# Kernel optimization log

Hardware: AMD Instinct MI355X
Metric: run time of the kernel (lower is better)

## Reference

```python
import jax, jax.numpy as jnp
import numpy as np

LUT_N = 16 * 17 * 17 * 17  # 78608, covers max index 16*(16*17*17 + 16*17 + 16) = 78592
H = W = 2048


def setup_inputs() -> dict:
    key = jax.random.key(0)
    k1, k2, k3, k4 = jax.random.split(key, 4)
    # quantized pixel values in [0, 16], stored as float like the torch module expects
    x_in = jax.random.randint(k1, (1, 3, H, W), 0, 17).astype(jnp.float32)
    x_s = jax.random.randint(k2, (1, 3, H, W), 0, 17).astype(jnp.float32)
    # int8 LUT tables of shape [N, 20, 1, 1]
    feature_msb = jax.random.randint(k3, (LUT_N, 20, 1, 1), -32, 32).astype(jnp.int8)
    feature_lsb = jax.random.randint(k4, (LUT_N, 20, 1, 1), -32, 32).astype(jnp.int8)
    return {"x_in": x_in, "x_s": x_s, "feature_msb": feature_msb, "feature_lsb": feature_lsb}


def reference(x_in, x_s, feature_msb, feature_lsb):
    B, C, Hh, Ww = x_in.shape
    # index weights: [16*17*17, 16*17, 16], broadcast over (1,3,1,1)
    weights = jnp.array([16 * 17 * 17, 16 * 17, 16], dtype=jnp.float32).reshape(1, 3, 1, 1)
    idx_msb = jnp.sum(x_in * weights, axis=1).reshape(-1).astype(jnp.int32)  # [B*H*W]
    idx_lsb = jnp.sum(x_s * weights, axis=1).reshape(-1).astype(jnp.int32)
    nfeat = feature_msb.shape[1]  # 20
    # gather -> (1, H, W, 20) -> (1, 20, H, W), cast to float as in torch .float()
    out_msb = feature_msb[idx_msb].reshape(1, Hh, Ww, nfeat).transpose(0, 3, 1, 2).astype(jnp.float32)
    out_lsb = feature_lsb[idx_lsb].reshape(1, Hh, Ww, nfeat).transpose(0, 3, 1, 2).astype(jnp.float32)
    out = out_msb + out_lsb
    # AdaptiveAvgPool2d(1) == global mean over H, W
    out = jnp.mean(out, axis=(2, 3), keepdims=True)  # (1, 20, 1, 1)
    # quantize to 0.25 steps and clamp to [-32, 31.75]
    out = jnp.clip(jnp.round(out * 4.0) / 4.0, -32.0, 31.75)
    return out
```

## Files before the change

kernel.cpp:

```cpp
#include <hip/hip_runtime.h>


#define NBINS 4913
#define NPIX  (2048 * 2048)
#define G4    (NPIX / 4)
#define NFEAT 20

__global__ __launch_bounds__(256) void compact_k(const int* __restrict__ msb,
                                                 const int* __restrict__ lsb,
                                                 int* __restrict__ cm,
                                                 int* __restrict__ cl) {
    int ok = 1;
    for (int i = 0; i < 64; ++i) {
        int v = msb[i];
        ok &= (v >= -32 && v < 32);
    }
    const bool is_int32 = (ok != 0);

    const int total = NBINS * 5;
    int t = blockIdx.x * 256 + threadIdx.x;
    const int stride = gridDim.x * 256;
    for (; t < total; t += stride) {
        int j = t / 5;
        int k = t - j * 5;
        int wm, wl;
        if (is_int32) {
            const int* rm = msb + j * 320 + k * 4;
            const int* rl = lsb + j * 320 + k * 4;
            unsigned um = (unsigned)(rm[0] & 0xff) | ((unsigned)(rm[1] & 0xff) << 8) |
                          ((unsigned)(rm[2] & 0xff) << 16) | ((unsigned)(rm[3] & 0xff) << 24);
            unsigned ul = (unsigned)(rl[0] & 0xff) | ((unsigned)(rl[1] & 0xff) << 8) |
                          ((unsigned)(rl[2] & 0xff) << 16) | ((unsigned)(rl[3] & 0xff) << 24);
            wm = (int)um;
            wl = (int)ul;
        } else {
            wm = msb[j * 80 + k];
            wl = lsb[j * 80 + k];
        }
        cm[t] = wm;
        cl[t] = wl;
    }
}

__global__ __launch_bounds__(256) void feat_main(const float* __restrict__ xin,
                                                 const float* __restrict__ xs,
                                                 const int* __restrict__ cm,
                                                 const int* __restrict__ cl,
                                                 int* __restrict__ partial) {
    __shared__ int hist[NBINS];
    __shared__ int wsum[4][NFEAT];
    for (int i = threadIdx.x; i < NBINS; i += 256) hist[i] = 0;
    __syncthreads();

    const float4* a = (const float4*)xin;
    const float4* b = (const float4*)xs;
    const int nt = gridDim.x * 256;
    for (int g = blockIdx.x * 256 + threadIdx.x; g < G4; g += nt) {
        float4 a0 = a[g], a1 = a[g + G4], a2 = a[g + 2 * G4];
        float4 b0 = b[g], b1 = b[g + G4], b2 = b[g + 2 * G4];

        int m0 = (int)fmaf(a0.x, 289.0f, fmaf(a1.x, 17.0f, a2.x));
        int m1 = (int)fmaf(a0.y, 289.0f, fmaf(a1.y, 17.0f, a2.y));
        int m2 = (int)fmaf(a0.z, 289.0f, fmaf(a1.z, 17.0f, a2.z));
        int m3 = (int)fmaf(a0.w, 289.0f, fmaf(a1.w, 17.0f, a2.w));
        int s0 = (int)fmaf(b0.x, 289.0f, fmaf(b1.x, 17.0f, b2.x));
        int s1 = (int)fmaf(b0.y, 289.0f, fmaf(b1.y, 17.0f, b2.y));
        int s2 = (int)fmaf(b0.z, 289.0f, fmaf(b1.z, 17.0f, b2.z));
        int s3 = (int)fmaf(b0.w, 289.0f, fmaf(b1.w, 17.0f, b2.w));

        atomicAdd(&hist[m0], 1);
        atomicAdd(&hist[m1], 1);
        atomicAdd(&hist[m2], 1);
        atomicAdd(&hist[m3], 1);
        atomicAdd(&hist[s0], 1 << 16);
        atomicAdd(&hist[s1], 1 << 16);
        atomicAdd(&hist[s2], 1 << 16);
        atomicAdd(&hist[s3], 1 << 16);
    }
    __syncthreads();

    int acc[NFEAT];
#pragma unroll
    for (int f = 0; f < NFEAT; ++f) acc[f] = 0;

    for (int j = threadIdx.x; j < NBINS; j += 256) {
        int h = hist[j];
        int hm = h & 0xffff;
        int hl = (int)((unsigned)h >> 16);
        if (hm) {
            const int* r = cm + j * 5;
#pragma unroll
            for (int k = 0; k < 5; ++k) {
                int w = r[k];
                acc[4 * k + 0] += hm * ((w << 24) >> 24);
                acc[4 * k + 1] += hm * ((w << 16) >> 24);
                acc[4 * k + 2] += hm * ((w << 8) >> 24);
                acc[4 * k + 3] += hm * (w >> 24);
            }
        }
        if (hl) {
            const int* r = cl + j * 5;
#pragma unroll
            for (int k = 0; k < 5; ++k) {
                int w = r[k];
                acc[4 * k + 0] += hl * ((w << 24) >> 24);
                acc[4 * k + 1] += hl * ((w << 16) >> 24);
                acc[4 * k + 2] += hl * ((w << 8) >> 24);
                acc[4 * k + 3] += hl * (w >> 24);
            }
        }
    }

    const int lane = threadIdx.x & 63;
    const int wv = threadIdx.x >> 6;
#pragma unroll
    for (int f = 0; f < NFEAT; ++f) {
        int v = acc[f];
#pragma unroll
        for (int o = 32; o > 0; o >>= 1) v += __shfl_xor(v, o, 64);
        if (lane == 0) wsum[wv][f] = v;
    }
    __syncthreads();
    if (threadIdx.x < NFEAT) {
        int f = threadIdx.x;
        partial[blockIdx.x * NFEAT + f] = wsum[0][f] + wsum[1][f] + wsum[2][f] + wsum[3][f];
    }
}

__global__ __launch_bounds__(64) void finalize_k(const int* __restrict__ partial,
                                                 float* __restrict__ out, int nb) {
    const int f = blockIdx.x;
    const int lane = threadIdx.x;
    int s = 0;
    for (int b = lane; b < nb; b += 64) s += partial[b * NFEAT + f];
#pragma unroll
    for (int o = 32; o > 0; o >>= 1) s += __shfl_xor(s, o, 64);
    if (lane == 0) {
        double m4 = (double)s * (1.0 / 1048576.0);
        double r = rint(m4);
        float v = (float)(r * 0.25);
        v = fminf(fmaxf(v, -32.0f), 31.75f);
        out[f] = v;
    }
}

extern "C" void kernel_launch(void* const* d_in, const int* in_sizes, int n_in,
                              void* d_out, int out_size, void* d_ws, size_t ws_size,
                              hipStream_t stream) {
    const float* xin = (const float*)d_in[0];
    const float* xs = (const float*)d_in[1];
    const int* msb = (const int*)d_in[2];
    const int* lsb = (const int*)d_in[3];
    float* out = (float*)d_out;

    int* cm = (int*)d_ws;
    int* cl = (int*)((char*)d_ws + 98304);
    int* partial = (int*)((char*)d_ws + 2 * 98304);

    const int mb = (ws_size >= (size_t)(2 * 98304) + 2048u * NFEAT * 4u) ? 2048 : 1024;

    compact_k<<<96, 256, 0, stream>>>(msb, lsb, cm, cl);
    feat_main<<<mb, 256, 0, stream>>>(xin, xs, cm, cl, partial);
    finalize_k<<<NFEAT, 64, 0, stream>>>(partial, out, mb);
}
```

Before: 169.8 us.

## Merge per-block histograms globally before LUT dot product

Each histogram block now writes its shared-memory histogram to a global workspace row instead of multiplying it against the LUT itself. A separate merge kernel sums the histograms across blocks per bin and does the 20-feature dot product once per bin. This replaces 2048 redundant per-block dot products over 4913 bins with one. The cost is an extra kernel launch and roughly 40 MB of histogram traffic written and read back. The old fused path is kept as a fallback when the workspace is too small.

```diff
diff --git a/kernel.cpp b/kernel.cpp
--- a/kernel.cpp
+++ b/kernel.cpp
@@ -2,9 +2,14 @@
 
 
 #define NBINS 4913
+#define HPAD  4928
 #define NPIX  (2048 * 2048)
 #define G4    (NPIX / 4)
 #define NFEAT 20
+#define MERGE_BLOCKS 154
+
+#define PART_OFF 196608
+#define HIST_OFF 278528
 
 __global__ __launch_bounds__(256) void compact_k(const int* __restrict__ msb,
                                                  const int* __restrict__ lsb,
@@ -42,13 +47,10 @@
     }
 }
 
-__global__ __launch_bounds__(256) void feat_main(const float* __restrict__ xin,
+__global__ __launch_bounds__(256) void feat_hist(const float* __restrict__ xin,
                                                  const float* __restrict__ xs,
-                                                 const int* __restrict__ cm,
-                                                 const int* __restrict__ cl,
-                                                 int* __restrict__ partial) {
+                                                 unsigned* __restrict__ hists) {
     __shared__ int hist[NBINS];
-    __shared__ int wsum[4][NFEAT];
     for (int i = threadIdx.x; i < NBINS; i += 256) hist[i] = 0;
     __syncthreads();
 
@@ -79,10 +81,102 @@
     }
     __syncthreads();
 
+    unsigned* row = hists + (size_t)blockIdx.x * HPAD;
+    for (int i = threadIdx.x; i < HPAD; i += 256)
+        row[i] = (i < NBINS) ? (unsigned)hist[i] : 0u;
+}
+
+__global__ __launch_bounds__(256) void merge_dot_k(const unsigned* __restrict__ hists,
+                                                   const int* __restrict__ cm,
+                                                   const int* __restrict__ cl,
+                                                   int* __restrict__ partial, int nh) {
+    __shared__ unsigned part[8][32];
+    const int t = threadIdx.x;
+    const int s = t >> 5;
+    const int bo = t & 31;
+    const int j = blockIdx.x * 32 + bo;
+
+    unsigned sum = 0;
+    for (int b = s; b < nh; b += 8)
+        sum += hists[(size_t)b * HPAD + j];
+    part[s][bo] = sum;
+    __syncthreads();
+
+    if (t < 32) {
+        unsigned h = 0;
+#pragma unroll
+        for (int ss = 0; ss < 8; ++ss) h += part[ss][bo];
+        int hm = (int)(h & 0xffffu);
+        int hl = (int)(h >> 16);
+
+        int acc[NFEAT];
+#pragma unroll
+        for (int f = 0; f < NFEAT; ++f) acc[f] = 0;
+        if (j < NBINS && h != 0u) {
+            const int* rm = cm + j * 5;
+            const int* rl = cl + j * 5;
+#pragma unroll
+            for (int k = 0; k < 5; ++k) {
+                int wm = rm[k], wl = rl[k];
+                acc[4 * k + 0] += hm * ((wm << 24) >> 24) + hl * ((wl << 24) >> 24);
+                acc[4 * k + 1] += hm * ((wm << 16) >> 24) + hl * ((wl << 16) >> 24);
+                acc[4 * k + 2] += hm * ((wm << 8) >> 24) + hl * ((wl << 8) >> 24);
+                acc[4 * k + 3] += hm * (wm >> 24) + hl * (wl >> 24);
+            }
+        }
+#pragma unroll
+        for (int f = 0; f < NFEAT; ++f) {
+            int v = acc[f];
+#pragma unroll
+            for (int o = 16; o > 0; o >>= 1) v += __shfl_xor(v, o, 64);
+            acc[f] = v;
+        }
+        if (t == 0) {
+#pragma unroll
+            for (int f = 0; f < NFEAT; ++f)
+                partial[blockIdx.x * NFEAT + f] = acc[f];
+        }
+    }
+}
+
+__global__ __launch_bounds__(256) void feat_dot(const float* __restrict__ xin,
+                                                const float* __restrict__ xs,
+                                                const int* __restrict__ cm,
+                                                const int* __restrict__ cl,
+                                                int* __restrict__ partial) {
+    __shared__ int hist[NBINS];
+    __shared__ int wsum[4][NFEAT];
+    for (int i = threadIdx.x; i < NBINS; i += 256) hist[i] = 0;
+    __syncthreads();
+
+    const float4* a = (const float4*)xin;
+    const float4* b = (const float4*)xs;
+    const int nt = gridDim.x * 256;
+    for (int g = blockIdx.x * 256 + threadIdx.x; g < G4; g += nt) {
+        float4 a0 = a[g], a1 = a[g + G4], a2 = a[g + 2 * G4];
+        float4 b0 = b[g], b1 = b[g + G4], b2 = b[g + 2 * G4];
+        int m0 = (int)fmaf(a0.x, 289.0f, fmaf(a1.x, 17.0f, a2.x));
+        int m1 = (int)fmaf(a0.y, 289.0f, fmaf(a1.y, 17.0f, a2.y));
+        int m2 = (int)fmaf(a0.z, 289.0f, fmaf(a1.z, 17.0f, a2.z));
+        int m3 = (int)fmaf(a0.w, 289.0f, fmaf(a1.w, 17.0f, a2.w));
+        int s0 = (int)fmaf(b0.x, 289.0f, fmaf(b1.x, 17.0f, b2.x));
+        int s1 = (int)fmaf(b0.y, 289.0f, fmaf(b1.y, 17.0f, b2.y));
+        int s2 = (int)fmaf(b0.z, 289.0f, fmaf(b1.z, 17.0f, b2.z));
+        int s3 = (int)fmaf(b0.w, 289.0f, fmaf(b1.w, 17.0f, b2.w));
+        atomicAdd(&hist[m0], 1);
+        atomicAdd(&hist[m1], 1);
+        atomicAdd(&hist[m2], 1);
+        atomicAdd(&hist[m3], 1);
+        atomicAdd(&hist[s0], 1 << 16);
+        atomicAdd(&hist[s1], 1 << 16);
+        atomicAdd(&hist[s2], 1 << 16);
+        atomicAdd(&hist[s3], 1 << 16);
+    }
+    __syncthreads();
+
     int acc[NFEAT];
 #pragma unroll
     for (int f = 0; f < NFEAT; ++f) acc[f] = 0;
-
     for (int j = threadIdx.x; j < NBINS; j += 256) {
         int h = hist[j];
         int hm = h & 0xffff;
@@ -155,11 +249,21 @@
 
     int* cm = (int*)d_ws;
     int* cl = (int*)((char*)d_ws + 98304);
-    int* partial = (int*)((char*)d_ws + 2 * 98304);
-
-    const int mb = (ws_size >= (size_t)(2 * 98304) + 2048u * NFEAT * 4u) ? 2048 : 1024;
+    int* partial = (int*)((char*)d_ws + PART_OFF);
+    unsigned* hists = (unsigned*)((char*)d_ws + HIST_OFF);
+
+    const size_t rowb = (size_t)HPAD * 4;
+    int nh = 0;
+    if (ws_size >= (size_t)HIST_OFF + 2048 * rowb) nh = 2048;
+    else if (ws_size >= (size_t)HIST_OFF + 1024 * rowb) nh = 1024;
 
     compact_k<<<96, 256, 0, stream>>>(msb, lsb, cm, cl);
-    feat_main<<<mb, 256, 0, stream>>>(xin, xs, cm, cl, partial);
-    finalize_k<<<NFEAT, 64, 0, stream>>>(partial, out, mb);
-}
+    if (nh) {
+        feat_hist<<<nh, 256, 0, stream>>>(xin, xs, hists);
+        merge_dot_k<<<MERGE_BLOCKS, 256, 0, stream>>>(hists, cm, cl, partial, nh);
+        finalize_k<<<NFEAT, 64, 0, stream>>>(partial, out, MERGE_BLOCKS);
+    } else {
+        feat_dot<<<1024, 256, 0, stream>>>(xin, xs, cm, cl, partial);
+        finalize_k<<<NFEAT, 64, 0, stream>>>(partial, out, 1024);
+    }
+}
```

Measured after the change: 184.3 us. 8.5% more time.
